# Kernel optimization log

Measured on AMD Instinct MI355X. Metric: run time of the kernel, lower is better.

## Reference

```python
import jax, jax.numpy as jnp
import numpy as np

N, F, H = 1024, 512, 64
SPARSITY_WEIGHT = 0.01


def setup_inputs() -> dict:
    key = jax.random.key(0)
    ks = jax.random.split(key, 9)
    s = lambda fan_in: 1.0 / np.sqrt(fan_in)
    return {
        "node_features": jax.random.normal(ks[0], (N, F), dtype=jnp.float32),
        # node_transform: Linear(F->H), ReLU, Linear(H->H)
        "W1": jax.random.uniform(ks[1], (F, H), jnp.float32, -s(F), s(F)),
        "b1": jax.random.uniform(ks[2], (H,), jnp.float32, -s(F), s(F)),
        "W2": jax.random.uniform(ks[3], (H, H), jnp.float32, -s(H), s(H)),
        "b2": jax.random.uniform(ks[4], (H,), jnp.float32, -s(H), s(H)),
        # attn: Linear(2H->H), ReLU, Linear(H->1)
        "Wa1": jax.random.uniform(ks[5], (2 * H, H), jnp.float32, -s(2 * H), s(2 * H)),
        "ba1": jax.random.uniform(ks[6], (H,), jnp.float32, -s(2 * H), s(2 * H)),
        "wa2": jax.random.uniform(ks[7], (H,), jnp.float32, -s(H), s(H)),
        "ba2": jax.random.uniform(ks[8], (), jnp.float32, -s(H), s(H)),
        "temperature": jnp.float32(1.0),
    }


def reference(node_features, W1, b1, W2, b2, Wa1, ba1, wa2, ba2, temperature):
    # node transform: h = Linear(ReLU(Linear(x)))  -> [N, H]
    h = jax.nn.relu(node_features @ W1 + b1) @ W2 + b2
    # attn(concat(h_i, h_j)) decomposed GAT-style:
    # concat([h_i, h_j]) @ Wa1 == h_i @ Wa1[:H] + h_j @ Wa1[H:]
    e_i = h @ Wa1[:H]   # [N, H]
    e_j = h @ Wa1[H:]   # [N, H]
    z = jax.nn.relu(e_i[:, None, :] + e_j[None, :, :] + ba1)  # [N, N, H]
    scores = jnp.einsum("ijh,h->ij", z, wa2) + ba2            # [N, N]
    scores = scores / jnp.clip(temperature, 0.1, 5.0)
    scores = (scores + scores.T) * 0.5
    adjacency = jax.nn.sigmoid(scores)
    sparsity_loss = SPARSITY_WEIGHT * jnp.mean(jnp.abs(adjacency))
    return (adjacency, sparsity_loss)
```

## Files before the change

### kernel.cpp

```cpp
#include <hip/hip_runtime.h>
#include <cmath>

#define NN 1024
#define FF 512
#define HH 64
#define NPAIRS 528

__global__ __launch_bounds__(1024, 4) void k1_transform(
    const float* __restrict__ x, const float* __restrict__ W1,
    const float* __restrict__ b1, const float* __restrict__ W2,
    const float* __restrict__ b2, const float* __restrict__ Wa1,
    const float* __restrict__ ba1,
    float* __restrict__ ei, float* __restrict__ ejb)
{
    __shared__ float xs[4][516];
    __shared__ float ts[4][68];
    __shared__ float hs[4][68];
    __shared__ float pp[16][4][68];
    const int tid = threadIdx.x;
    const int row0 = blockIdx.x * 4;

    if (tid < 512) {
        int r = tid >> 7;
        int cc = (tid & 127) << 2;
        *reinterpret_cast<float4*>(&xs[r][cc]) =
            *reinterpret_cast<const float4*>(x + (row0 + r) * FF + cc);
    }
    __syncthreads();

    const int ks = tid >> 6;
    const int r  = (tid >> 4) & 3;
    const int cg = (tid & 15) << 2;

    {
        float4 acc = make_float4(0.f, 0.f, 0.f, 0.f);
        const int k0 = ks * 32;
        #pragma unroll 4
        for (int k = k0; k < k0 + 32; k += 4) {
            float4 a  = *reinterpret_cast<const float4*>(&xs[r][k]);
            float4 w0 = *reinterpret_cast<const float4*>(W1 + (k + 0) * HH + cg);
            float4 w1 = *reinterpret_cast<const float4*>(W1 + (k + 1) * HH + cg);
            float4 w2 = *reinterpret_cast<const float4*>(W1 + (k + 2) * HH + cg);
            float4 w3 = *reinterpret_cast<const float4*>(W1 + (k + 3) * HH + cg);
            acc.x += a.x * w0.x + a.y * w1.x + a.z * w2.x + a.w * w3.x;
            acc.y += a.x * w0.y + a.y * w1.y + a.z * w2.y + a.w * w3.y;
            acc.z += a.x * w0.z + a.y * w1.z + a.z * w2.z + a.w * w3.z;
            acc.w += a.x * w0.w + a.y * w1.w + a.z * w2.w + a.w * w3.w;
        }
        *reinterpret_cast<float4*>(&pp[ks][r][cg]) = acc;
    }
    __syncthreads();
    if (ks == 0) {
        float4 s0 = *reinterpret_cast<const float4*>(&pp[0][r][cg]);
        #pragma unroll
        for (int q = 1; q < 16; ++q) {
            float4 p = *reinterpret_cast<const float4*>(&pp[q][r][cg]);
            s0.x += p.x; s0.y += p.y; s0.z += p.z; s0.w += p.w;
        }
        float4 bv = *reinterpret_cast<const float4*>(b1 + cg);
        float4 t;
        t.x = fmaxf(s0.x + bv.x, 0.f);
        t.y = fmaxf(s0.y + bv.y, 0.f);
        t.z = fmaxf(s0.z + bv.z, 0.f);
        t.w = fmaxf(s0.w + bv.w, 0.f);
        *reinterpret_cast<float4*>(&ts[r][cg]) = t;
    }
    __syncthreads();

    {
        float4 acc = make_float4(0.f, 0.f, 0.f, 0.f);
        const int k = ks * 4;
        float4 a  = *reinterpret_cast<const float4*>(&ts[r][k]);
        float4 w0 = *reinterpret_cast<const float4*>(W2 + (k + 0) * HH + cg);
        float4 w1 = *reinterpret_cast<const float4*>(W2 + (k + 1) * HH + cg);
        float4 w2 = *reinterpret_cast<const float4*>(W2 + (k + 2) * HH + cg);
        float4 w3 = *reinterpret_cast<const float4*>(W2 + (k + 3) * HH + cg);
        acc.x += a.x * w0.x + a.y * w1.x + a.z * w2.x + a.w * w3.x;
        acc.y += a.x * w0.y + a.y * w1.y + a.z * w2.y + a.w * w3.y;
        acc.z += a.x * w0.z + a.y * w1.z + a.z * w2.z + a.w * w3.z;
        acc.w += a.x * w0.w + a.y * w1.w + a.z * w2.w + a.w * w3.w;
        *reinterpret_cast<float4*>(&pp[ks][r][cg]) = acc;
    }
    __syncthreads();
    if (ks == 0) {
        float4 s0 = *reinterpret_cast<const float4*>(&pp[0][r][cg]);
        #pragma unroll
        for (int q = 1; q < 16; ++q) {
            float4 p = *reinterpret_cast<const float4*>(&pp[q][r][cg]);
            s0.x += p.x; s0.y += p.y; s0.z += p.z; s0.w += p.w;
        }
        float4 bv = *reinterpret_cast<const float4*>(b2 + cg);
        float4 h;
        h.x = s0.x + bv.x; h.y = s0.y + bv.y;
        h.z = s0.z + bv.z; h.w = s0.w + bv.w;
        *reinterpret_cast<float4*>(&hs[r][cg]) = h;
    }
    __syncthreads();

    {
        const float* Wb = Wa1 + (ks >> 3) * HH * HH;
        float4 acc = make_float4(0.f, 0.f, 0.f, 0.f);
        const int k0 = (ks & 7) * 8;
        #pragma unroll
        for (int k = k0; k < k0 + 8; k += 4) {
            float4 a  = *reinterpret_cast<const float4*>(&hs[r][k]);
            float4 w0 = *reinterpret_cast<const float4*>(Wb + (k + 0) * HH + cg);
            float4 w1 = *reinterpret_cast<const float4*>(Wb + (k + 1) * HH + cg);
            float4 w2 = *reinterpret_cast<const float4*>(Wb + (k + 2) * HH + cg);
            float4 w3 = *reinterpret_cast<const float4*>(Wb + (k + 3) * HH + cg);
            acc.x += a.x * w0.x + a.y * w1.x + a.z * w2.x + a.w * w3.x;
            acc.y += a.x * w0.y + a.y * w1.y + a.z * w2.y + a.w * w3.y;
            acc.z += a.x * w0.z + a.y * w1.z + a.z * w2.z + a.w * w3.z;
            acc.w += a.x * w0.w + a.y * w1.w + a.z * w2.w + a.w * w3.w;
        }
        *reinterpret_cast<float4*>(&pp[ks][r][cg]) = acc;
    }
    __syncthreads();
    if (ks == 0) {
        float4 s0 = *reinterpret_cast<const float4*>(&pp[0][r][cg]);
        #pragma unroll
        for (int q = 1; q < 8; ++q) {
            float4 p = *reinterpret_cast<const float4*>(&pp[q][r][cg]);
            s0.x += p.x; s0.y += p.y; s0.z += p.z; s0.w += p.w;
        }
        *reinterpret_cast<float4*>(ei + (row0 + r) * HH + cg) = s0;
    } else if (ks == 8) {
        float4 s0 = *reinterpret_cast<const float4*>(&pp[8][r][cg]);
        #pragma unroll
        for (int q = 9; q < 16; ++q) {
            float4 p = *reinterpret_cast<const float4*>(&pp[q][r][cg]);
            s0.x += p.x; s0.y += p.y; s0.z += p.z; s0.w += p.w;
        }
        float4 bv = *reinterpret_cast<const float4*>(ba1 + cg);
        s0.x += bv.x; s0.y += bv.y; s0.z += bv.z; s0.w += bv.w;
        *reinterpret_cast<float4*>(ejb + (row0 + r) * HH + cg) = s0;
    }
}

__global__ __launch_bounds__(512, 2) void k2_raw(
    const float* __restrict__ ei, const float* __restrict__ ejb,
    const float* __restrict__ wa2, float* __restrict__ sraw)
{
    __shared__ float eil[64][68];
    __shared__ float ejl[64][68];
    __shared__ float wl[64];
    const int tid = threadIdx.x;
    const int i0 = (blockIdx.x >> 4) * 64;
    const int j0 = (blockIdx.x & 15) * 64;

    {
        const int rr = tid >> 4;
        const int cq = (tid & 15) << 2;
        #pragma unroll
        for (int l = 0; l < 2; ++l) {
            int r = rr + 32 * l;
            *reinterpret_cast<float4*>(&eil[r][cq]) =
                *reinterpret_cast<const float4*>(ei + (i0 + r) * HH + cq);
            *reinterpret_cast<float4*>(&ejl[r][cq]) =
                *reinterpret_cast<const float4*>(ejb + (j0 + r) * HH + cq);
        }
    }
    if (tid < 16) {
        *reinterpret_cast<float4*>(&wl[tid * 4]) =
            *reinterpret_cast<const float4*>(wa2 + tid * 4);
    }
    __syncthreads();

    const int ty = tid >> 5;
    const int tx = tid & 31;
    float acc[4][2] = {};

    #pragma unroll 4
    for (int h = 0; h < HH; h += 4) {
        float4 w  = *reinterpret_cast<const float4*>(&wl[h]);
        float4 B0 = *reinterpret_cast<const float4*>(&ejl[tx][h]);
        float4 B1 = *reinterpret_cast<const float4*>(&ejl[tx + 32][h]);
        #pragma unroll
        for (int m = 0; m < 4; ++m) {
            float4 A = *reinterpret_cast<const float4*>(&eil[ty + 16 * m][h]);
            acc[m][0] += fmaxf(A.x + B0.x, 0.f) * w.x
                       + fmaxf(A.y + B0.y, 0.f) * w.y
                       + fmaxf(A.z + B0.z, 0.f) * w.z
                       + fmaxf(A.w + B0.w, 0.f) * w.w;
            acc[m][1] += fmaxf(A.x + B1.x, 0.f) * w.x
                       + fmaxf(A.y + B1.y, 0.f) * w.y
                       + fmaxf(A.z + B1.z, 0.f) * w.z
                       + fmaxf(A.w + B1.w, 0.f) * w.w;
        }
    }
    #pragma unroll
    for (int m = 0; m < 4; ++m) {
        const int row = i0 + ty + 16 * m;
        sraw[row * NN + j0 + tx]      = acc[m][0];
        sraw[row * NN + j0 + tx + 32] = acc[m][1];
    }
}

__global__ __launch_bounds__(256, 4) void k3_sym(
    float* __restrict__ s, const float* __restrict__ ba2,
    const float* __restrict__ temp, float* __restrict__ partials)
{
    __shared__ float A[32][36];
    __shared__ float Bt[32][33];
    __shared__ float wsum[4];
    const int tid = threadIdx.x;

    int I = 0, rem = blockIdx.x, rl = 32;
    while (rem >= rl) { rem -= rl; ++I; --rl; }
    const int J = I + rem;
    const int bi = I * 32, bj = J * 32;
    const bool off = (I != J);

    const int rb = tid >> 3;
    const int cb = (tid & 7) << 2;

    {
        *reinterpret_cast<float4*>(&A[rb][cb]) =
            *reinterpret_cast<const float4*>(s + (bi + rb) * NN + bj + cb);
        float4 bv = *reinterpret_cast<const float4*>(s + (bj + rb) * NN + bi + cb);
        Bt[cb + 0][rb] = bv.x;
        Bt[cb + 1][rb] = bv.y;
        Bt[cb + 2][rb] = bv.z;
        Bt[cb + 3][rb] = bv.w;
    }
    __syncthreads();

    const float t = fminf(fmaxf(temp[0], 0.1f), 5.0f);
    const float invt = 1.0f / t;
    const float bb = ba2[0];

    float vals[4];
    float lsum = 0.f;
    #pragma unroll
    for (int e = 0; e < 4; ++e) {
        const int c = cb + e;
        float v = (0.5f * (A[rb][c] + Bt[rb][c]) + bb) * invt;
        float adj = 1.0f / (1.0f + __expf(-v));
        vals[e] = adj;
        lsum += adj;
    }
    __syncthreads();

    {
        float4 o;
        o.x = vals[0]; o.y = vals[1]; o.z = vals[2]; o.w = vals[3];
        *reinterpret_cast<float4*>(s + (bi + rb) * NN + bj + cb) = o;
        A[rb][cb + 0] = vals[0];
        A[rb][cb + 1] = vals[1];
        A[rb][cb + 2] = vals[2];
        A[rb][cb + 3] = vals[3];
    }

    if (off) {
        __syncthreads();
        float4 o;
        o.x = A[cb + 0][rb];
        o.y = A[cb + 1][rb];
        o.z = A[cb + 2][rb];
        o.w = A[cb + 3][rb];
        *reinterpret_cast<float4*>(s + (bj + rb) * NN + bi + cb) = o;
        lsum *= 2.0f;
    }

    float w = lsum;
    #pragma unroll
    for (int o = 32; o > 0; o >>= 1) w += __shfl_down(w, o);
    if ((tid & 63) == 0) wsum[tid >> 6] = w;
    __syncthreads();
    if (tid == 0) {
        partials[blockIdx.x] = (wsum[0] + wsum[1]) + (wsum[2] + wsum[3]);
    }
}

__global__ __launch_bounds__(256) void k4_reduce(
    const float* __restrict__ partials, float* __restrict__ out_loss)
{
    __shared__ float wsum[4];
    const int tid = threadIdx.x;
    float v = partials[tid] + partials[tid + 256];
    if (tid < 16) v += partials[tid + 512];
    #pragma unroll
    for (int o = 32; o > 0; o >>= 1) v += __shfl_down(v, o);
    if ((tid & 63) == 0) wsum[tid >> 6] = v;
    __syncthreads();
    if (tid == 0) {
        float tot = (wsum[0] + wsum[1]) + (wsum[2] + wsum[3]);
        *out_loss = 0.01f * tot / (float)(NN * NN);
    }
}

extern "C" void kernel_launch(void* const* d_in, const int* in_sizes, int n_in,
                              void* d_out, int out_size, void* d_ws, size_t ws_size,
                              hipStream_t stream)
{
    const float* x    = (const float*)d_in[0];
    const float* W1   = (const float*)d_in[1];
    const float* b1   = (const float*)d_in[2];
    const float* W2   = (const float*)d_in[3];
    const float* b2   = (const float*)d_in[4];
    const float* Wa1  = (const float*)d_in[5];
    const float* ba1  = (const float*)d_in[6];
    const float* wa2  = (const float*)d_in[7];
    const float* ba2  = (const float*)d_in[8];
    const float* temp = (const float*)d_in[9];
    float* out = (float*)d_out;

    float* ei    = (float*)d_ws;
    float* ejb   = ei + NN * HH;
    float* parts = ejb + NN * HH;

    k1_transform<<<NN / 4, 1024, 0, stream>>>(x, W1, b1, W2, b2, Wa1, ba1, ei, ejb);
    k2_raw<<<256, 512, 0, stream>>>(ei, ejb, wa2, out);
    k3_sym<<<NPAIRS, 256, 0, stream>>>(out, ba2, temp, parts);
    k4_reduce<<<1, 256, 0, stream>>>(parts, out + NN * NN);
}
```

Baseline: 27.37 us.

## Rewrite ReLU score as abs plus linear terms and retile pairwise kernel

The pairwise score kernel now uses relu(x) = 0.5*(|x| + x). It accumulates |a+b|*w in the inner loop and adds per-row and per-column linear dot products (ei·wa2, ejb·wa2), computed once per tile, at the end. This replaces max+mul with abs folded into the FMA as a source modifier, aiming to save an instruction per element. The tile also changes from 64x64 with 512 threads to 64x32 with 256 threads over 512 blocks, which adds an extra sync and a small dot-product phase.

```diff
diff --git a/kernel.cpp b/kernel.cpp
--- a/kernel.cpp
+++ b/kernel.cpp
@@ -137,28 +137,34 @@
     }
 }
 
-__global__ __launch_bounds__(512, 2) void k2_raw(
+__global__ __launch_bounds__(256, 4) void k2_raw(
     const float* __restrict__ ei, const float* __restrict__ ejb,
     const float* __restrict__ wa2, float* __restrict__ sraw)
 {
     __shared__ float eil[64][68];
-    __shared__ float ejl[64][68];
+    __shared__ float ejl[32][68];
     __shared__ float wl[64];
+    __shared__ float li[64];
+    __shared__ float lj[32];
     const int tid = threadIdx.x;
-    const int i0 = (blockIdx.x >> 4) * 64;
-    const int j0 = (blockIdx.x & 15) * 64;
-
-    {
-        const int rr = tid >> 4;
-        const int cq = (tid & 15) << 2;
-        #pragma unroll
-        for (int l = 0; l < 2; ++l) {
-            int r = rr + 32 * l;
-            *reinterpret_cast<float4*>(&eil[r][cq]) =
-                *reinterpret_cast<const float4*>(ei + (i0 + r) * HH + cq);
-            *reinterpret_cast<float4*>(&ejl[r][cq]) =
-                *reinterpret_cast<const float4*>(ejb + (j0 + r) * HH + cq);
-        }
+    const int i0 = (blockIdx.x >> 5) * 64;
+    const int j0 = (blockIdx.x & 31) * 32;
+
+    #pragma unroll
+    for (int l = 0; l < 4; ++l) {
+        int f4 = tid + l * 256;
+        int r = f4 >> 4;
+        int c = (f4 & 15) << 2;
+        *reinterpret_cast<float4*>(&eil[r][c]) =
+            *reinterpret_cast<const float4*>(ei + (i0 + r) * HH + c);
+    }
+    #pragma unroll
+    for (int l = 0; l < 2; ++l) {
+        int f4 = tid + l * 256;
+        int r = f4 >> 4;
+        int c = (f4 & 15) << 2;
+        *reinterpret_cast<float4*>(&ejl[r][c]) =
+            *reinterpret_cast<const float4*>(ejb + (j0 + r) * HH + c);
     }
     if (tid < 16) {
         *reinterpret_cast<float4*>(&wl[tid * 4]) =
@@ -166,33 +172,55 @@
     }
     __syncthreads();
 
-    const int ty = tid >> 5;
-    const int tx = tid & 31;
+    if (tid < 192) {
+        const int row  = tid >> 1;
+        const int half = tid & 1;
+        const float* src = (row < 64) ? &eil[row][0] : &ejl[row - 64][0];
+        float sdot = 0.f;
+        const int h0 = half * 32;
+        #pragma unroll
+        for (int h = h0; h < h0 + 32; h += 4) {
+            float4 v = *reinterpret_cast<const float4*>(&src[h]);
+            float4 w = *reinterpret_cast<const float4*>(&wl[h]);
+            sdot += v.x * w.x + v.y * w.y + v.z * w.z + v.w * w.w;
+        }
+        sdot += __shfl_xor(sdot, 1);
+        if (half == 0) {
+            if (row < 64) li[row] = sdot;
+            else          lj[row - 64] = sdot;
+        }
+    }
+    __syncthreads();
+
+    const int ty = tid >> 4;
+    const int tx = tid & 15;
     float acc[4][2] = {};
 
     #pragma unroll 4
     for (int h = 0; h < HH; h += 4) {
         float4 w  = *reinterpret_cast<const float4*>(&wl[h]);
         float4 B0 = *reinterpret_cast<const float4*>(&ejl[tx][h]);
-        float4 B1 = *reinterpret_cast<const float4*>(&ejl[tx + 32][h]);
+        float4 B1 = *reinterpret_cast<const float4*>(&ejl[tx + 16][h]);
         #pragma unroll
         for (int m = 0; m < 4; ++m) {
             float4 A = *reinterpret_cast<const float4*>(&eil[ty + 16 * m][h]);
-            acc[m][0] += fmaxf(A.x + B0.x, 0.f) * w.x
-                       + fmaxf(A.y + B0.y, 0.f) * w.y
-                       + fmaxf(A.z + B0.z, 0.f) * w.z
-                       + fmaxf(A.w + B0.w, 0.f) * w.w;
-            acc[m][1] += fmaxf(A.x + B1.x, 0.f) * w.x
-                       + fmaxf(A.y + B1.y, 0.f) * w.y
-                       + fmaxf(A.z + B1.z, 0.f) * w.z
-                       + fmaxf(A.w + B1.w, 0.f) * w.w;
+            acc[m][0] += __builtin_fabsf(A.x + B0.x) * w.x
+                       + __builtin_fabsf(A.y + B0.y) * w.y
+                       + __builtin_fabsf(A.z + B0.z) * w.z
+                       + __builtin_fabsf(A.w + B0.w) * w.w;
+            acc[m][1] += __builtin_fabsf(A.x + B1.x) * w.x
+                       + __builtin_fabsf(A.y + B1.y) * w.y
+                       + __builtin_fabsf(A.z + B1.z) * w.z
+                       + __builtin_fabsf(A.w + B1.w) * w.w;
         }
     }
     #pragma unroll
     for (int m = 0; m < 4; ++m) {
-        const int row = i0 + ty + 16 * m;
-        sraw[row * NN + j0 + tx]      = acc[m][0];
-        sraw[row * NN + j0 + tx + 32] = acc[m][1];
+        const int rloc = ty + 16 * m;
+        const int row  = i0 + rloc;
+        const float l0 = li[rloc];
+        sraw[row * NN + j0 + tx]      = 0.5f * (acc[m][0] + l0 + lj[tx]);
+        sraw[row * NN + j0 + tx + 16] = 0.5f * (acc[m][1] + l0 + lj[tx + 16]);
     }
 }
 
@@ -310,7 +338,7 @@
     float* parts = ejb + NN * HH;
 
     k1_transform<<<NN / 4, 1024, 0, stream>>>(x, W1, b1, W2, b2, Wa1, ba1, ei, ejb);
-    k2_raw<<<256, 512, 0, stream>>>(ei, ejb, wa2, out);
+    k2_raw<<<512, 256, 0, stream>>>(ei, ejb, wa2, out);
     k3_sym<<<NPAIRS, 256, 0, stream>>>(out, ba2, temp, parts);
     k4_reduce<<<1, 256, 0, stream>>>(parts, out + NN * NN);
 }
```

New measurement: 27.22 us. No clear change (-0.6%).
